# Kernel tuning notes

Measured on AMD Instinct MI355X. Metric: run time of the kernel, lower is better.

Reference implementation:

```python
import jax, jax.numpy as jnp
import numpy as np

N, C, L, E, H = 2000, 4, 5000, 64000, 512
REP = 207  # length after conv front-end: floor((floor((5000-11)/4)+1 - 11)/6)+1


def setup_inputs() -> dict:
    key = jax.random.key(0)
    ks = jax.random.split(key, 10)

    def init(k, shape, fan_in):
        return jax.random.normal(k, shape, jnp.float32) / np.sqrt(fan_in).astype(np.float32)

    x = jax.random.normal(ks[0], (N, C, L), jnp.float32)
    edge_index = jax.random.randint(ks[1], (2, E), 0, N)
    return dict(
        x=x, edge_index=edge_index,
        w1=init(ks[2], (16, C, 1), C), b1=jnp.zeros(16, jnp.float32),
        w2=init(ks[3], (4, 4, 11), 4 * 11), b2=jnp.zeros(4, jnp.float32),
        w3=init(ks[4], (1, 4, 11), 4 * 11), b3=jnp.zeros(1, jnp.float32),
        gcn_w=init(ks[5], (REP, H), REP), gcn_b=jnp.zeros(H, jnp.float32),
        lin_w=init(ks[6], (REP, H), REP), lin_b=jnp.zeros(H, jnp.float32),
        gate_w=init(ks[7], (H, H), H), gate_b=jnp.zeros(H, jnp.float32),
        bn_gamma=jnp.ones(H, jnp.float32), bn_beta=jnp.zeros(H, jnp.float32),
    )


def _conv1d(x, w, b, stride):
    # x: [N, Cin, L], w: [Cout, Cin, K] (torch OIH layout), VALID padding
    y = jax.lax.conv_general_dilated(x, w, (stride,), 'VALID',
                                     dimension_numbers=('NCH', 'OIH', 'NCH'))
    return y + b[None, :, None]


def _gcn_conv(feat, edge_index, w, b, n):
    # GCNConv: x@W, add self-loops, sym-normalize, scatter-add, + bias
    h = feat @ w                                      # [N, H]
    loops = jnp.arange(n)
    src = jnp.concatenate([edge_index[0], loops])
    dst = jnp.concatenate([edge_index[1], loops])
    deg = jax.ops.segment_sum(jnp.ones_like(src, h.dtype), dst, num_segments=n)
    dinv = jax.lax.rsqrt(deg)                         # deg >= 1 due to self-loops
    norm = dinv[src] * dinv[dst]                      # [E+N]
    out = jax.ops.segment_sum(h[src] * norm[:, None], dst, num_segments=n)
    return out + b


def reference(x, edge_index, w1, b1, w2, b2, w3, b3,
              gcn_w, gcn_b, lin_w, lin_b, gate_w, gate_b, bn_gamma, bn_beta):
    n = x.shape[0]
    # conv front-end (dropout layers are identity at inference)
    h = jax.nn.relu(_conv1d(x, w1, b1, 1))            # [N, 16, L]
    # MaxPool1d(k=4,s=4) applied on permuted [N, L, 16] == pool over channel dim
    h = h.reshape(n, 4, 4, L).max(axis=2)             # [N, 4, L]
    h = jax.nn.relu(_conv1d(h, w2, b2, 4))            # [N, 4, 1248]
    h = jax.nn.relu(_conv1d(h, w3, b3, 6))            # [N, 1, 207]
    feat = h[:, 0, :]                                 # squeeze -> [N, REP]
    # GCN + gated fusion
    z = jnp.tanh(_gcn_conv(feat, edge_index, gcn_w, gcn_b, n))
    g = jax.nn.sigmoid(z @ gate_w + gate_b)
    xl = feat @ lin_w + lin_b
    out = jax.nn.relu((1.0 - g) * xl + g * z)
    # BatchNorm over node dim (batch statistics, training-mode semantics)
    mean = out.mean(axis=0)
    var = out.var(axis=0)
    out = (out - mean) * jax.lax.rsqrt(var + 1e-5) * bn_gamma + bn_beta
    return out
```

## Files before the change

### kernel.cpp

```cpp
#include <hip/hip_runtime.h>
#include <hip/hip_bf16.h>
#include <cstddef>

#define NN 2000
#define CC 4
#define LL1 5000
#define LL2 1248
#define LL3 207
#define HH 512
#define EE 64000

__device__ float g_feat[NN * LL3];
__device__ float g_aggf[NN * LL3];
__device__ float g_z[NN * HH];
__device__ float g_xl[NN * HH];
__device__ float g_obuf[NN * HH];
__device__ float g_dinv[NN];
__device__ float g_colsum[HH];
__device__ float g_colsq[HH];
__device__ float g_sc[HH];
__device__ float g_sh[HH];
__device__ int   g_cnt[NN];
__device__ int   g_cursor[NN];
__device__ int   g_off[NN];
__device__ int   g_bucket[EE];

__global__ void zero_init() {
    int i = blockIdx.x * 256 + threadIdx.x;
    if (i < NN) { g_cnt[i] = 0; g_cursor[i] = 0; }
    if (i < HH) { g_colsum[i] = 0.f; g_colsq[i] = 0.f; }
}

#define MCH 1256
__global__ __launch_bounds__(256) void conv_chain(
    const float* __restrict__ x,
    const float* __restrict__ w1, const float* __restrict__ b1,
    const float* __restrict__ w2, const float* __restrict__ b2,
    const float* __restrict__ w3, const float* __restrict__ b3)
{
    __shared__ __align__(16) float sm[4 * MCH];
    __shared__ __align__(16) float sy[4 * LL2];

    const int tid = threadIdx.x;
    const int node = blockIdx.x;
    const float* xb = x + (size_t)node * (CC * LL1);

    float w1r[64], b1r[16];
#pragma unroll
    for (int i = 0; i < 64; ++i) w1r[i] = w1[i];
#pragma unroll
    for (int i = 0; i < 16; ++i) b1r[i] = b1[i];

#pragma unroll 1
    for (int c = 0; c < 4; ++c) {
        const int l0 = 1248 * c;
        for (int g4 = tid; g4 < 314; g4 += 256) {
            const int l = l0 + 4 * g4;
            float xs[4][4];
#pragma unroll
            for (int ch = 0; ch < 4; ++ch)
                *(float4*)xs[ch] = *(const float4*)(xb + ch * LL1 + l);
#pragma unroll
            for (int g = 0; g < 4; ++g) {
                float mv[4];
#pragma unroll
                for (int li = 0; li < 4; ++li) {
                    float best = -1e30f;
#pragma unroll
                    for (int j = 0; j < 4; ++j) {
                        int o = g * 4 + j;
                        float v = b1r[o] + w1r[o*4+0]*xs[0][li] + w1r[o*4+1]*xs[1][li]
                                         + w1r[o*4+2]*xs[2][li] + w1r[o*4+3]*xs[3][li];
                        best = fmaxf(best, v);
                    }
                    mv[li] = fmaxf(best, 0.f);
                }
                *(float4*)&sm[g * MCH + 4 * g4] = make_float4(mv[0], mv[1], mv[2], mv[3]);
            }
        }
        __syncthreads();

        const int T0 = 312 * c;
#pragma unroll 1
        for (int pair = 0; pair < 2; ++pair) {
            const float* wp = w2 + 88 * pair;
            float wo[88];
#pragma unroll
            for (int i = 0; i < 88; ++i) wo[i] = wp[i];
            const float bo0 = b2[2 * pair], bo1 = b2[2 * pair + 1];
            for (int T = tid; T < 312; T += 256) {
                float a0 = bo0, a1 = bo1;
#pragma unroll
                for (int i = 0; i < 4; ++i) {
                    const float* mp = sm + i * MCH + 4 * T;
                    float4 u0 = *(const float4*)mp;
                    float4 u1 = *(const float4*)(mp + 4);
                    float4 u2 = *(const float4*)(mp + 8);
                    float v[12] = {u0.x, u0.y, u0.z, u0.w,
                                   u1.x, u1.y, u1.z, u1.w,
                                   u2.x, u2.y, u2.z, u2.w};
#pragma unroll
                    for (int k = 0; k < 11; ++k) {
                        a0 += wo[i * 11 + k] * v[k];
                        a1 += wo[44 + i * 11 + k] * v[k];
                    }
                }
                sy[(2 * pair) * LL2 + T0 + T]     = fmaxf(a0, 0.f);
                sy[(2 * pair + 1) * LL2 + T0 + T] = fmaxf(a1, 0.f);
            }
        }
        __syncthreads();
    }

    if (tid < LL3) {
        float acc = b3[0];
#pragma unroll
        for (int i = 0; i < 4; ++i)
#pragma unroll
            for (int k = 0; k < 11; ++k)
                acc += w3[i * 11 + k] * sy[i * LL2 + 6 * tid + k];
        g_feat[(size_t)node * LL3 + tid] = fmaxf(acc, 0.f);
    }
}

__global__ void edge_count(const int* __restrict__ ei, int E) {
    int e = blockIdx.x * 256 + threadIdx.x;
    if (e < E) atomicAdd(&g_cnt[ei[E + e]], 1);
}

__global__ __launch_bounds__(256) void scan_dinv() {
    __shared__ int a[2048], b[2048];
    int tid = threadIdx.x;
    for (int i = tid; i < 2048; i += 256) a[i] = (i < NN) ? g_cnt[i] : 0;
    __syncthreads();
    int* src = a; int* dst = b;
    for (int d = 1; d < 2048; d <<= 1) {
        for (int i = tid; i < 2048; i += 256)
            dst[i] = src[i] + ((i >= d) ? src[i - d] : 0);
        __syncthreads();
        int* t = src; src = dst; dst = t;
    }
    for (int i = tid; i < NN; i += 256) {
        g_off[i] = src[i] - g_cnt[i];
        g_dinv[i] = rsqrtf(1.0f + (float)g_cnt[i]);
    }
}

__global__ void bucket_fill(const int* __restrict__ ei, int E) {
    int e = blockIdx.x * 256 + threadIdx.x;
    if (e < E) {
        int d = ei[E + e];
        int p = atomicAdd(&g_cursor[d], 1);
        g_bucket[g_off[d] + p] = ei[e];
    }
}

__global__ __launch_bounds__(256) void agg_feat() {
    const int d = blockIdx.x;
    const int tid = threadIdx.x;
    if (tid >= LL3) return;
    const float di = g_dinv[d];
    const int nb = g_cnt[d];
    const int base = g_off[d];
    float acc = g_feat[(size_t)d * LL3 + tid] * di;
    int j = 0;
    for (; j + 1 < nb; j += 2) {
        int s0 = g_bucket[base + j];
        int s1 = g_bucket[base + j + 1];
        acc += g_feat[(size_t)s0 * LL3 + tid] * g_dinv[s0]
             + g_feat[(size_t)s1 * LL3 + tid] * g_dinv[s1];
    }
    if (j < nb) {
        int s = g_bucket[base + j];
        acc += g_feat[(size_t)s * LL3 + tid] * g_dinv[s];
    }
    g_aggf[(size_t)d * LL3 + tid] = acc * di;
}

template<int EPI>
__global__ __launch_bounds__(256) void gemm64(
    const float* __restrict__ A, const float* __restrict__ B,
    const float* __restrict__ bias, float* __restrict__ C,
    const float* __restrict__ xl, const float* __restrict__ zb,
    int M, int N, int K)
{
    __shared__ float As[2][16][64];
    __shared__ float Bs[2][16][64];
    __shared__ float rs[64], rq[64];
    const int tid = threadIdx.x;
    const int N0 = blockIdx.x * 64, M0 = blockIdx.y * 64;
    const int tx = tid & 15, ty = tid >> 4;
    const int ar = tid & 63, ac = (tid >> 6) * 4;
    const int bk = tid >> 4, bn = (tid & 15) * 4;
    const int NT = (K + 15) / 16;

    float acc[4][4] = {};
    float ra[4]; float4 rb;

    {
        int r = M0 + ar;
#pragma unroll
        for (int q = 0; q < 4; ++q) {
            int kk = ac + q;
            ra[q] = (r < M && kk < K) ? A[(size_t)r * K + kk] : 0.f;
        }
        rb = (bk < K) ? *(const float4*)(B + (size_t)bk * N + N0 + bn) : make_float4(0,0,0,0);
#pragma unroll
        for (int q = 0; q < 4; ++q) As[0][ac + q][ar] = ra[q];
        *(float4*)&Bs[0][bk][bn] = rb;
    }
    __syncthreads();

#pragma unroll 1
    for (int kt = 0; kt < NT; ++kt) {
        const int cur = kt & 1;
        if (kt + 1 < NT) {
            int k0 = (kt + 1) * 16;
            int r = M0 + ar;
#pragma unroll
            for (int q = 0; q < 4; ++q) {
                int kk = k0 + ac + q;
                ra[q] = (r < M && kk < K) ? A[(size_t)r * K + kk] : 0.f;
            }
            int kb = k0 + bk;
            rb = (kb < K) ? *(const float4*)(B + (size_t)kb * N + N0 + bn) : make_float4(0,0,0,0);
        }
#pragma unroll
        for (int k = 0; k < 16; ++k) {
            float4 a4 = *(const float4*)&As[cur][k][ty * 4];
            float4 b4 = *(const float4*)&Bs[cur][k][tx * 4];
            acc[0][0] += a4.x * b4.x; acc[0][1] += a4.x * b4.y; acc[0][2] += a4.x * b4.z; acc[0][3] += a4.x * b4.w;
            acc[1][0] += a4.y * b4.x; acc[1][1] += a4.y * b4.y; acc[1][2] += a4.y * b4.z; acc[1][3] += a4.y * b4.w;
            acc[2][0] += a4.z * b4.x; acc[2][1] += a4.z * b4.y; acc[2][2] += a4.z * b4.z; acc[2][3] += a4.z * b4.w;
            acc[3][0] += a4.w * b4.x; acc[3][1] += a4.w * b4.y; acc[3][2] += a4.w * b4.z; acc[3][3] += a4.w * b4.w;
        }
        if (kt + 1 < NT) {
            const int nxt = cur ^ 1;
#pragma unroll
            for (int q = 0; q < 4; ++q) As[nxt][ac + q][ar] = ra[q];
            *(float4*)&Bs[nxt][bk][bn] = rb;
        }
        __syncthreads();
    }

    const int c0 = N0 + tx * 4;
    float4 bb4 = bias ? *(const float4*)(bias + c0) : make_float4(0,0,0,0);
    float bb[4] = {bb4.x, bb4.y, bb4.z, bb4.w};

    if (EPI == 2) {
        float cs[4] = {0,0,0,0}, cq[4] = {0,0,0,0};
#pragma unroll
        for (int i = 0; i < 4; ++i) {
            int r = M0 + ty * 4 + i;
            if (r < M) {
                float4 xv = *(const float4*)(xl + (size_t)r * N + c0);
                float4 zv = *(const float4*)(zb + (size_t)r * N + c0);
                float xa[4] = {xv.x, xv.y, xv.z, xv.w};
                float za[4] = {zv.x, zv.y, zv.z, zv.w};
                float va[4];
#pragma unroll
                for (int j = 0; j < 4; ++j) {
                    float g = 1.f / (1.f + __expf(-(acc[i][j] + bb[j])));
                    float v = fmaxf((1.f - g) * xa[j] + g * za[j], 0.f);
                    va[j] = v; cs[j] += v; cq[j] += v * v;
                }
                *(float4*)(C + (size_t)r * N + c0) = make_float4(va[0], va[1], va[2], va[3]);
            }
        }
        if (tid < 64) { rs[tid] = 0.f; rq[tid] = 0.f; }
        __syncthreads();
#pragma unroll
        for (int j = 0; j < 4; ++j) {
            atomicAdd(&rs[tx * 4 + j], cs[j]);
            atomicAdd(&rq[tx * 4 + j], cq[j]);
        }
        __syncthreads();
        if (tid < 64) {
            atomicAdd(&g_colsum[N0 + tid], rs[tid]);
            atomicAdd(&g_colsq[N0 + tid], rq[tid]);
        }
    } else {
#pragma unroll
        for (int i = 0; i < 4; ++i) {
            int r = M0 + ty * 4 + i;
            if (r < M) {
                float va[4];
#pragma unroll
                for (int j = 0; j < 4; ++j) {
                    float v = acc[i][j] + bb[j];
                    if (EPI == 1) v = tanhf(v);
                    va[j] = v;
                }
                *(float4*)(C + (size_t)r * N + c0) = make_float4(va[0], va[1], va[2], va[3]);
            }
        }
    }
}

__global__ void bn_stats(const float* __restrict__ gamma, const float* __restrict__ beta) {
    int c = threadIdx.x;
    float mean = g_colsum[c] * (1.f / (float)NN);
    float var = g_colsq[c] * (1.f / (float)NN) - mean * mean;
    float s = rsqrtf(var + 1e-5f) * gamma[c];
    g_sc[c] = s;
    g_sh[c] = beta[c] - mean * s;
}

__global__ __launch_bounds__(256) void bn_apply(float* __restrict__ out) {
    int i = blockIdx.x * 256 + threadIdx.x;
    int c = i & (HH - 1);
    out[i] = g_obuf[i] * g_sc[c] + g_sh[c];
}

extern "C" void kernel_launch(void* const* d_in, const int* in_sizes, int n_in,
                              void* d_out, int out_size, void* d_ws, size_t ws_size,
                              hipStream_t stream) {
    (void)d_ws; (void)ws_size; (void)n_in; (void)out_size;
    const float* x      = (const float*)d_in[0];
    const int*   ei     = (const int*)d_in[1];
    const float* w1     = (const float*)d_in[2];
    const float* b1     = (const float*)d_in[3];
    const float* w2     = (const float*)d_in[4];
    const float* b2     = (const float*)d_in[5];
    const float* w3     = (const float*)d_in[6];
    const float* b3     = (const float*)d_in[7];
    const float* gcn_w  = (const float*)d_in[8];
    const float* gcn_b  = (const float*)d_in[9];
    const float* lin_w  = (const float*)d_in[10];
    const float* lin_b  = (const float*)d_in[11];
    const float* gate_w = (const float*)d_in[12];
    const float* gate_b = (const float*)d_in[13];
    const float* bn_g   = (const float*)d_in[14];
    const float* bn_b   = (const float*)d_in[15];
    float* out = (float*)d_out;
    const int E = in_sizes[1] / 2;

    float* feat = nullptr; float* aggf = nullptr; float* z = nullptr;
    float* xl = nullptr; float* obuf = nullptr;
    hipGetSymbolAddress((void**)&feat, HIP_SYMBOL(g_feat));
    hipGetSymbolAddress((void**)&aggf, HIP_SYMBOL(g_aggf));
    hipGetSymbolAddress((void**)&z,    HIP_SYMBOL(g_z));
    hipGetSymbolAddress((void**)&xl,   HIP_SYMBOL(g_xl));
    hipGetSymbolAddress((void**)&obuf, HIP_SYMBOL(g_obuf));

    zero_init<<<8, 256, 0, stream>>>();
    conv_chain<<<NN, 256, 0, stream>>>(x, w1, b1, w2, b2, w3, b3);
    edge_count<<<(E + 255) / 256, 256, 0, stream>>>(ei, E);
    scan_dinv<<<1, 256, 0, stream>>>();
    bucket_fill<<<(E + 255) / 256, 256, 0, stream>>>(ei, E);
    agg_feat<<<NN, 256, 0, stream>>>();

    dim3 gg(HH / 64, (NN + 63) / 64);
    gemm64<1><<<gg, 256, 0, stream>>>(aggf, gcn_w, gcn_b, z, nullptr, nullptr, NN, HH, LL3);
    gemm64<0><<<gg, 256, 0, stream>>>(feat, lin_w, lin_b, xl, nullptr, nullptr, NN, HH, LL3);
    gemm64<2><<<gg, 256, 0, stream>>>(z, gate_w, gate_b, obuf, xl, z, NN, HH, HH);

    bn_stats<<<1, HH, 0, stream>>>(bn_g, bn_b);
    bn_apply<<<(NN * HH) / 256, 256, 0, stream>>>(out);
}
```

Baseline: 386.1 us.

## Pad feature stride, vectorize aggregation, merge GEMMs with smaller tiles, fold BN stats

Feature rows are padded to a stride of 208 so that the neighbour aggregation can use float4 loads, with four nodes handled per block. The two K=207 GEMMs become a single launch over a z-dimension, and all GEMMs move from 64x64 to 32x32 tiles to create more blocks for the GPU's many CUs. This trades register reuse per thread for higher occupancy and parallelism. The separate bn_stats kernel is removed, and each bn_apply thread now recomputes its column's scale and shift.

```diff
diff --git a/kernel.cpp b/kernel.cpp
--- a/kernel.cpp
+++ b/kernel.cpp
@@ -7,19 +7,18 @@
 #define LL1 5000
 #define LL2 1248
 #define LL3 207
+#define FSTR 208
 #define HH 512
 #define EE 64000
 
-__device__ float g_feat[NN * LL3];
-__device__ float g_aggf[NN * LL3];
+__device__ float g_feat[NN * FSTR];
+__device__ float g_aggf[NN * FSTR];
 __device__ float g_z[NN * HH];
 __device__ float g_xl[NN * HH];
 __device__ float g_obuf[NN * HH];
 __device__ float g_dinv[NN];
 __device__ float g_colsum[HH];
 __device__ float g_colsq[HH];
-__device__ float g_sc[HH];
-__device__ float g_sh[HH];
 __device__ int   g_cnt[NN];
 __device__ int   g_cursor[NN];
 __device__ int   g_off[NN];
@@ -112,14 +111,18 @@
         __syncthreads();
     }
 
-    if (tid < LL3) {
-        float acc = b3[0];
-#pragma unroll
-        for (int i = 0; i < 4; ++i)
-#pragma unroll
-            for (int k = 0; k < 11; ++k)
-                acc += w3[i * 11 + k] * sy[i * LL2 + 6 * tid + k];
-        g_feat[(size_t)node * LL3 + tid] = fmaxf(acc, 0.f);
+    if (tid < FSTR) {
+        float acc = 0.f;
+        if (tid < LL3) {
+            acc = b3[0];
+#pragma unroll
+            for (int i = 0; i < 4; ++i)
+#pragma unroll
+                for (int k = 0; k < 11; ++k)
+                    acc += w3[i * 11 + k] * sy[i * LL2 + 6 * tid + k];
+            acc = fmaxf(acc, 0.f);
+        }
+        g_feat[(size_t)node * FSTR + tid] = acc;
     }
 }
 
@@ -156,160 +159,188 @@
 }
 
 __global__ __launch_bounds__(256) void agg_feat() {
-    const int d = blockIdx.x;
-    const int tid = threadIdx.x;
-    if (tid >= LL3) return;
+    const int sub = threadIdx.x >> 6;
+    const int lane = threadIdx.x & 63;
+    const int d = blockIdx.x * 4 + sub;
+    if (lane >= 52) return;
     const float di = g_dinv[d];
     const int nb = g_cnt[d];
     const int base = g_off[d];
-    float acc = g_feat[(size_t)d * LL3 + tid] * di;
+    const size_t co = (size_t)lane * 4;
+    float4 a = *(const float4*)(g_feat + (size_t)d * FSTR + co);
+    float ax = a.x * di, ay = a.y * di, az = a.z * di, aw = a.w * di;
     int j = 0;
     for (; j + 1 < nb; j += 2) {
         int s0 = g_bucket[base + j];
         int s1 = g_bucket[base + j + 1];
-        acc += g_feat[(size_t)s0 * LL3 + tid] * g_dinv[s0]
-             + g_feat[(size_t)s1 * LL3 + tid] * g_dinv[s1];
+        float w0 = g_dinv[s0], w1 = g_dinv[s1];
+        float4 f0 = *(const float4*)(g_feat + (size_t)s0 * FSTR + co);
+        float4 f1 = *(const float4*)(g_feat + (size_t)s1 * FSTR + co);
+        ax += f0.x * w0 + f1.x * w1;
+        ay += f0.y * w0 + f1.y * w1;
+        az += f0.z * w0 + f1.z * w1;
+        aw += f0.w * w0 + f1.w * w1;
     }
     if (j < nb) {
         int s = g_bucket[base + j];
-        acc += g_feat[(size_t)s * LL3 + tid] * g_dinv[s];
-    }
-    g_aggf[(size_t)d * LL3 + tid] = acc * di;
-}
-
-template<int EPI>
-__global__ __launch_bounds__(256) void gemm64(
-    const float* __restrict__ A, const float* __restrict__ B,
-    const float* __restrict__ bias, float* __restrict__ C,
-    const float* __restrict__ xl, const float* __restrict__ zb,
-    int M, int N, int K)
+        float w = g_dinv[s];
+        float4 f = *(const float4*)(g_feat + (size_t)s * FSTR + co);
+        ax += f.x * w; ay += f.y * w; az += f.z * w; aw += f.w * w;
+    }
+    *(float4*)(g_aggf + (size_t)d * FSTR + co) = make_float4(ax * di, ay * di, az * di, aw * di);
+}
+
+__global__ __launch_bounds__(256) void gemm_zxl(
+    const float* __restrict__ gcn_w, const float* __restrict__ gcn_b,
+    const float* __restrict__ lin_w, const float* __restrict__ lin_b)
 {
-    __shared__ float As[2][16][64];
-    __shared__ float Bs[2][16][64];
-    __shared__ float rs[64], rq[64];
+    __shared__ float As[2][16][33];
+    __shared__ float Bs[2][16][32];
     const int tid = threadIdx.x;
-    const int N0 = blockIdx.x * 64, M0 = blockIdx.y * 64;
-    const int tx = tid & 15, ty = tid >> 4;
-    const int ar = tid & 63, ac = (tid >> 6) * 4;
-    const int bk = tid >> 4, bn = (tid & 15) * 4;
-    const int NT = (K + 15) / 16;
-
-    float acc[4][4] = {};
-    float ra[4]; float4 rb;
-
-    {
-        int r = M0 + ar;
-#pragma unroll
-        for (int q = 0; q < 4; ++q) {
-            int kk = ac + q;
-            ra[q] = (r < M && kk < K) ? A[(size_t)r * K + kk] : 0.f;
-        }
-        rb = (bk < K) ? *(const float4*)(B + (size_t)bk * N + N0 + bn) : make_float4(0,0,0,0);
-#pragma unroll
-        for (int q = 0; q < 4; ++q) As[0][ac + q][ar] = ra[q];
-        *(float4*)&Bs[0][bk][bn] = rb;
-    }
+    const int which = blockIdx.z;
+    const float* __restrict__ A = which ? g_feat : g_aggf;
+    const float* __restrict__ B = which ? lin_w : gcn_w;
+    const float* __restrict__ bias = which ? lin_b : gcn_b;
+    float* __restrict__ C = which ? g_xl : g_z;
+    const int N0 = blockIdx.x * 32, M0 = blockIdx.y * 32;
+    const int lr = tid >> 4, lk = tid & 15;
+    const int bk = tid >> 4, bn = (tid & 15) * 2;
+    const int ty = tid >> 3, tx = tid & 7;
+
+    float acc[4] = {0.f, 0.f, 0.f, 0.f};
+    float ra0, ra1; float2 rbv;
+    const int r0 = M0 + lr, r1 = M0 + lr + 16;
+
+    ra0 = (r0 < NN) ? A[(size_t)r0 * FSTR + lk] : 0.f;
+    ra1 = (r1 < NN) ? A[(size_t)r1 * FSTR + lk] : 0.f;
+    rbv = (bk < LL3) ? *(const float2*)(B + (size_t)bk * HH + N0 + bn) : make_float2(0.f, 0.f);
+    As[0][lk][lr] = ra0; As[0][lk][lr + 16] = ra1;
+    Bs[0][bk][bn] = rbv.x; Bs[0][bk][bn + 1] = rbv.y;
     __syncthreads();
 
 #pragma unroll 1
-    for (int kt = 0; kt < NT; ++kt) {
+    for (int kt = 0; kt < 13; ++kt) {
         const int cur = kt & 1;
-        if (kt + 1 < NT) {
+        if (kt + 1 < 13) {
             int k0 = (kt + 1) * 16;
-            int r = M0 + ar;
-#pragma unroll
-            for (int q = 0; q < 4; ++q) {
-                int kk = k0 + ac + q;
-                ra[q] = (r < M && kk < K) ? A[(size_t)r * K + kk] : 0.f;
-            }
+            ra0 = (r0 < NN) ? A[(size_t)r0 * FSTR + k0 + lk] : 0.f;
+            ra1 = (r1 < NN) ? A[(size_t)r1 * FSTR + k0 + lk] : 0.f;
             int kb = k0 + bk;
-            rb = (kb < K) ? *(const float4*)(B + (size_t)kb * N + N0 + bn) : make_float4(0,0,0,0);
+            rbv = (kb < LL3) ? *(const float2*)(B + (size_t)kb * HH + N0 + bn) : make_float2(0.f, 0.f);
         }
 #pragma unroll
         for (int k = 0; k < 16; ++k) {
-            float4 a4 = *(const float4*)&As[cur][k][ty * 4];
+            float av = As[cur][k][ty];
             float4 b4 = *(const float4*)&Bs[cur][k][tx * 4];
-            acc[0][0] += a4.x * b4.x; acc[0][1] += a4.x * b4.y; acc[0][2] += a4.x * b4.z; acc[0][3] += a4.x * b4.w;
-            acc[1][0] += a4.y * b4.x; acc[1][1] += a4.y * b4.y; acc[1][2] += a4.y * b4.z; acc[1][3] += a4.y * b4.w;
-            acc[2][0] += a4.z * b4.x; acc[2][1] += a4.z * b4.y; acc[2][2] += a4.z * b4.z; acc[2][3] += a4.z * b4.w;
-            acc[3][0] += a4.w * b4.x; acc[3][1] += a4.w * b4.y; acc[3][2] += a4.w * b4.z; acc[3][3] += a4.w * b4.w;
-        }
-        if (kt + 1 < NT) {
+            acc[0] += av * b4.x; acc[1] += av * b4.y; acc[2] += av * b4.z; acc[3] += av * b4.w;
+        }
+        if (kt + 1 < 13) {
             const int nxt = cur ^ 1;
-#pragma unroll
-            for (int q = 0; q < 4; ++q) As[nxt][ac + q][ar] = ra[q];
-            *(float4*)&Bs[nxt][bk][bn] = rb;
-        }
-        __syncthreads();
-    }
-
+            As[nxt][lk][lr] = ra0; As[nxt][lk][lr + 16] = ra1;
+            Bs[nxt][bk][bn] = rbv.x; Bs[nxt][bk][bn + 1] = rbv.y;
+        }
+        __syncthreads();
+    }
+
+    const int r = M0 + ty;
+    if (r < NN) {
+        const int c0 = N0 + tx * 4;
+        float4 bb = *(const float4*)(bias + c0);
+        float4 v = make_float4(acc[0] + bb.x, acc[1] + bb.y, acc[2] + bb.z, acc[3] + bb.w);
+        if (which == 0) { v.x = tanhf(v.x); v.y = tanhf(v.y); v.z = tanhf(v.z); v.w = tanhf(v.w); }
+        *(float4*)(C + (size_t)r * HH + c0) = v;
+    }
+}
+
+__global__ __launch_bounds__(256) void gemm_gate(
+    const float* __restrict__ gate_w, const float* __restrict__ gate_b)
+{
+    __shared__ float As[2][16][33];
+    __shared__ float Bs[2][16][32];
+    __shared__ float rs[32], rq[32];
+    const int tid = threadIdx.x;
+    const float* __restrict__ A = g_z;
+    const int N0 = blockIdx.x * 32, M0 = blockIdx.y * 32;
+    const int lr = tid >> 4, lk = tid & 15;
+    const int bk = tid >> 4, bn = (tid & 15) * 2;
+    const int ty = tid >> 3, tx = tid & 7;
+
+    float acc[4] = {0.f, 0.f, 0.f, 0.f};
+    float ra0, ra1; float2 rbv;
+    const int r0 = M0 + lr, r1 = M0 + lr + 16;
+
+    ra0 = (r0 < NN) ? A[(size_t)r0 * HH + lk] : 0.f;
+    ra1 = (r1 < NN) ? A[(size_t)r1 * HH + lk] : 0.f;
+    rbv = *(const float2*)(gate_w + (size_t)bk * HH + N0 + bn);
+    As[0][lk][lr] = ra0; As[0][lk][lr + 16] = ra1;
+    Bs[0][bk][bn] = rbv.x; Bs[0][bk][bn + 1] = rbv.y;
+    __syncthreads();
+
+#pragma unroll 1
+    for (int kt = 0; kt < 32; ++kt) {
+        const int cur = kt & 1;
+        if (kt + 1 < 32) {
+            int k0 = (kt + 1) * 16;
+            ra0 = (r0 < NN) ? A[(size_t)r0 * HH + k0 + lk] : 0.f;
+            ra1 = (r1 < NN) ? A[(size_t)r1 * HH + k0 + lk] : 0.f;
+            rbv = *(const float2*)(gate_w + (size_t)(k0 + bk) * HH + N0 + bn);
+        }
+#pragma unroll
+        for (int k = 0; k < 16; ++k) {
+            float av = As[cur][k][ty];
+            float4 b4 = *(const float4*)&Bs[cur][k][tx * 4];
+            acc[0] += av * b4.x; acc[1] += av * b4.y; acc[2] += av * b4.z; acc[3] += av * b4.w;
+        }
+        if (kt + 1 < 32) {
+            const int nxt = cur ^ 1;
+            As[nxt][lk][lr] = ra0; As[nxt][lk][lr + 16] = ra1;
+            Bs[nxt][bk][bn] = rbv.x; Bs[nxt][bk][bn + 1] = rbv.y;
+        }
+        __syncthreads();
+    }
+
+    const int r = M0 + ty;
     const int c0 = N0 + tx * 4;
-    float4 bb4 = bias ? *(const float4*)(bias + c0) : make_float4(0,0,0,0);
-    float bb[4] = {bb4.x, bb4.y, bb4.z, bb4.w};
-
-    if (EPI == 2) {
-        float cs[4] = {0,0,0,0}, cq[4] = {0,0,0,0};
-#pragma unroll
-        for (int i = 0; i < 4; ++i) {
-            int r = M0 + ty * 4 + i;
-            if (r < M) {
-                float4 xv = *(const float4*)(xl + (size_t)r * N + c0);
-                float4 zv = *(const float4*)(zb + (size_t)r * N + c0);
-                float xa[4] = {xv.x, xv.y, xv.z, xv.w};
-                float za[4] = {zv.x, zv.y, zv.z, zv.w};
-                float va[4];
-#pragma unroll
-                for (int j = 0; j < 4; ++j) {
-                    float g = 1.f / (1.f + __expf(-(acc[i][j] + bb[j])));
-                    float v = fmaxf((1.f - g) * xa[j] + g * za[j], 0.f);
-                    va[j] = v; cs[j] += v; cq[j] += v * v;
-                }
-                *(float4*)(C + (size_t)r * N + c0) = make_float4(va[0], va[1], va[2], va[3]);
-            }
-        }
-        if (tid < 64) { rs[tid] = 0.f; rq[tid] = 0.f; }
-        __syncthreads();
+    float cs[4] = {0.f, 0.f, 0.f, 0.f}, cq[4] = {0.f, 0.f, 0.f, 0.f};
+    if (r < NN) {
+        float4 bb = *(const float4*)(gate_b + c0);
+        float4 xv = *(const float4*)(g_xl + (size_t)r * HH + c0);
+        float4 zv = *(const float4*)(g_z + (size_t)r * HH + c0);
+        float pre[4] = {acc[0] + bb.x, acc[1] + bb.y, acc[2] + bb.z, acc[3] + bb.w};
+        float xa[4] = {xv.x, xv.y, xv.z, xv.w};
+        float za[4] = {zv.x, zv.y, zv.z, zv.w};
+        float va[4];
 #pragma unroll
         for (int j = 0; j < 4; ++j) {
-            atomicAdd(&rs[tx * 4 + j], cs[j]);
-            atomicAdd(&rq[tx * 4 + j], cq[j]);
-        }
-        __syncthreads();
-        if (tid < 64) {
-            atomicAdd(&g_colsum[N0 + tid], rs[tid]);
-            atomicAdd(&g_colsq[N0 + tid], rq[tid]);
-        }
-    } else {
-#pragma unroll
-        for (int i = 0; i < 4; ++i) {
-            int r = M0 + ty * 4 + i;
-            if (r < M) {
-                float va[4];
-#pragma unroll
-                for (int j = 0; j < 4; ++j) {
-                    float v = acc[i][j] + bb[j];
-                    if (EPI == 1) v = tanhf(v);
-                    va[j] = v;
-                }
-                *(float4*)(C + (size_t)r * N + c0) = make_float4(va[0], va[1], va[2], va[3]);
-            }
-        }
-    }
-}
-
-__global__ void bn_stats(const float* __restrict__ gamma, const float* __restrict__ beta) {
-    int c = threadIdx.x;
+            float g = 1.f / (1.f + __expf(-pre[j]));
+            float v = fmaxf((1.f - g) * xa[j] + g * za[j], 0.f);
+            va[j] = v; cs[j] = v; cq[j] = v * v;
+        }
+        *(float4*)(g_obuf + (size_t)r * HH + c0) = make_float4(va[0], va[1], va[2], va[3]);
+    }
+    if (tid < 32) { rs[tid] = 0.f; rq[tid] = 0.f; }
+    __syncthreads();
+#pragma unroll
+    for (int j = 0; j < 4; ++j) {
+        atomicAdd(&rs[tx * 4 + j], cs[j]);
+        atomicAdd(&rq[tx * 4 + j], cq[j]);
+    }
+    __syncthreads();
+    if (tid < 32) {
+        atomicAdd(&g_colsum[N0 + tid], rs[tid]);
+        atomicAdd(&g_colsq[N0 + tid], rq[tid]);
+    }
+}
+
+__global__ __launch_bounds__(256) void bn_apply(const float* __restrict__ gamma,
+                                                const float* __restrict__ beta,
+                                                float* __restrict__ out) {
+    int i = blockIdx.x * 256 + threadIdx.x;
+    int c = i & (HH - 1);
     float mean = g_colsum[c] * (1.f / (float)NN);
     float var = g_colsq[c] * (1.f / (float)NN) - mean * mean;
     float s = rsqrtf(var + 1e-5f) * gamma[c];
-    g_sc[c] = s;
-    g_sh[c] = beta[c] - mean * s;
-}
-
-__global__ __launch_bounds__(256) void bn_apply(float* __restrict__ out) {
-    int i = blockIdx.x * 256 + threadIdx.x;
-    int c = i & (HH - 1);
-    out[i] = g_obuf[i] * g_sc[c] + g_sh[c];
+    out[i] = g_obuf[i] * s + (beta[c] - mean * s);
 }
 
 extern "C" void kernel_launch(void* const* d_in, const int* in_sizes, int n_in,
@@ -335,26 +366,15 @@
     float* out = (float*)d_out;
     const int E = in_sizes[1] / 2;
 
-    float* feat = nullptr; float* aggf = nullptr; float* z = nullptr;
-    float* xl = nullptr; float* obuf = nullptr;
-    hipGetSymbolAddress((void**)&feat, HIP_SYMBOL(g_feat));
-    hipGetSymbolAddress((void**)&aggf, HIP_SYMBOL(g_aggf));
-    hipGetSymbolAddress((void**)&z,    HIP_SYMBOL(g_z));
-    hipGetSymbolAddress((void**)&xl,   HIP_SYMBOL(g_xl));
-    hipGetSymbolAddress((void**)&obuf, HIP_SYMBOL(g_obuf));
-
     zero_init<<<8, 256, 0, stream>>>();
     conv_chain<<<NN, 256, 0, stream>>>(x, w1, b1, w2, b2, w3, b3);
     edge_count<<<(E + 255) / 256, 256, 0, stream>>>(ei, E);
     scan_dinv<<<1, 256, 0, stream>>>();
     bucket_fill<<<(E + 255) / 256, 256, 0, stream>>>(ei, E);
-    agg_feat<<<NN, 256, 0, stream>>>();
-
-    dim3 gg(HH / 64, (NN + 63) / 64);
-    gemm64<1><<<gg, 256, 0, stream>>>(aggf, gcn_w, gcn_b, z, nullptr, nullptr, NN, HH, LL3);
-    gemm64<0><<<gg, 256, 0, stream>>>(feat, lin_w, lin_b, xl, nullptr, nullptr, NN, HH, LL3);
-    gemm64<2><<<gg, 256, 0, stream>>>(z, gate_w, gate_b, obuf, xl, z, NN, HH, HH);
-
-    bn_stats<<<1, HH, 0, stream>>>(bn_g, bn_b);
-    bn_apply<<<(NN * HH) / 256, 256, 0, stream>>>(out);
-}
+    agg_feat<<<NN / 4, 256, 0, stream>>>();
+
+    gemm_zxl<<<dim3(HH / 32, (NN + 31) / 32, 2), 256, 0, stream>>>(gcn_w, gcn_b, lin_w, lin_b);
+    gemm_gate<<<dim3(HH / 32, (NN + 31) / 32), 256, 0, stream>>>(gate_w, gate_b);
+
+    bn_apply<<<(NN * HH) / 256, 256, 0, stream>>>(bn_g, bn_b, out);
+}
```

New measurement: 384.6 us. Within noise of the previous version (-0.4%).
